# Kernel tuning notes

Measured on AMD Instinct MI355X. Metric: run time of the kernel, lower is better.

## Reference

```python
import jax, jax.numpy as jnp
import numpy as np

HEADS = 8

def setup_inputs() -> dict:
    key = jax.random.key(0)
    k1, k2 = jax.random.split(key)
    f_s = jax.random.normal(k1, (8, 256, 32, 32), dtype=jnp.float32)
    f_t = jax.random.normal(k2, (8, 256, 32, 32), dtype=jnp.float32)
    return {"f_s": f_s, "f_t": f_t}

def _to_tokens(x, heads):
    # 'b (h d) x y -> b h (x y) d'
    b, c, h, w = x.shape
    d = c // heads
    return x.reshape(b, heads, d, h * w).transpose(0, 1, 3, 2)

def reference(f_s, f_t):
    b, c, h, w = f_s.shape
    q = _to_tokens(f_s, HEADS)   # [b, H, n, d]
    k = _to_tokens(f_t, HEADS)
    v = _to_tokens(f_s, HEADS)
    # unscaled QK^T softmax V (faithful to source: no 1/sqrt(d) scaling)
    sim = jnp.einsum('bhid,bhjd->bhij', q, k)          # [b, H, n, n]
    attn = jax.nn.softmax(sim, axis=-1)
    out = jnp.einsum('bhij,bhjd->bhid', attn, v)       # [b, H, n, d]
    # 'b h (x y) d -> b (h d) x y'
    out = out.transpose(0, 1, 3, 2).reshape(b, c, h, w)
    loss = jnp.mean((out - f_t) ** 2)
    return loss
```

## Files before the change

kernel.cpp:

```cpp
#include <hip/hip_runtime.h>
#include <hip/hip_bf16.h>


typedef __attribute__((ext_vector_type(4))) float f32x4;
typedef __attribute__((ext_vector_type(16))) float f32x16;
typedef __attribute__((ext_vector_type(8))) short bf16x8;
typedef __attribute__((ext_vector_type(4))) unsigned u32x4;

#define KOFF 0
#define VOFF 65536
#define QOFF 131072
#define REDX 40960

__device__ __forceinline__ unsigned cvtpk(float a, float b) {
    unsigned r;
    asm("v_cvt_pk_bf16_f32 %0, %1, %2" : "=v"(r) : "v"(a), "v"(b));
    return r;
}
#define SWAP32(a, b) asm("v_permlane32_swap_b32 %0, %1" : "+v"(a), "+v"(b))

__device__ __forceinline__ float expv(float x) {
    float r;
    asm("v_exp_f32 %0, %1" : "=v"(r) : "v"(x));
    return r;
}

__global__ __launch_bounds__(512, 2)
void attn_mse_kernel(const float* __restrict__ fs, const float* __restrict__ ft,
                     float* __restrict__ out)
{
    __shared__ __align__(16) unsigned char smem[147456];

    const int tid  = threadIdx.x;
    const int lane = tid & 63;
    const int w    = tid >> 6;
    const int g    = lane >> 4;
    const int c    = lane & 15;
    const int il   = lane & 31;
    const int hi   = lane >> 5;

    const int bid  = blockIdx.x;
    const int pair = (bid & 7) * 8 + ((bid >> 3) & 7);
    const int q0   = (bid >> 6) * 256;

    const float* qb = fs + (size_t)pair * 32768;
    const float* kb = ft + (size_t)pair * 32768;

    const int p_ = c >> 2, jq = c & 3;
    const int dp = 4 * p_ + g;
    const int w0 = p_ * 64 + 16 * jq + 4 * (0 ^ p_) + g;
    const int w1 = p_ * 64 + 16 * jq + 4 * (1 ^ p_) + g;
    const int w2 = p_ * 64 + 16 * jq + 4 * (2 ^ p_) + g;
    const int w3 = p_ * 64 + 16 * jq + 4 * (3 ^ p_) + g;

    {
        const float sc = 1.44269504f;
        #pragma unroll
        for (int st = 0; st < 2; ++st) {
            const float* r0 = qb + (size_t)(2 * dp) * 1024 + (q0 + w * 32 + st * 16) + 4 * jq;
            const float4 a = *(const float4*)(r0);
            const float4 b = *(const float4*)(r0 + 1024);
            unsigned* dst = (unsigned*)(smem + QOFF + w * 2048 + st * 1024);
            dst[w0] = cvtpk(a.x * sc, b.x * sc);
            dst[w1] = cvtpk(a.y * sc, b.y * sc);
            dst[w2] = cvtpk(a.z * sc, b.z * sc);
            dst[w3] = cvtpk(a.w * sc, b.w * sc);
        }
    }
    const unsigned qsel = ((unsigned)(il >> 4) << 10) | (((unsigned)(il >> 2) & 3) << 6);
    const unsigned char* qbase = smem + QOFF + w * 2048 + qsel;
    const bf16x8 qfa = *(const bf16x8*)(qbase + ((hi << 8) | (((il & 3) ^ hi) << 4)));
    const bf16x8 qfb = *(const bf16x8*)(qbase + (((2 + hi) << 8) | (((il & 3) ^ (2 + hi)) << 4)));

    #pragma unroll
    for (int st = 0; st < 8; ++st) {
        const float* r0 = kb + (size_t)(2 * dp) * 1024 + (w * 128 + st * 16) + 4 * jq;
        const float4 a = *(const float4*)(r0);
        const float4 b = *(const float4*)(r0 + 1024);
        unsigned* dst = (unsigned*)(smem + KOFF + (w * 8 + st) * 1024);
        dst[w0] = cvtpk(a.x, b.x);
        dst[w1] = cvtpk(a.y, b.y);
        dst[w2] = cvtpk(a.z, b.z);
        dst[w3] = cvtpk(a.w, b.w);
    }
    {
        const int dv = w * 4 + g;
        #pragma unroll
        for (int tt = 0; tt < 16; ++tt) {
            const float4 vv = *(const float4*)(qb + (size_t)dv * 1024 + tt * 64 + 4 * c);
            const unsigned lo = cvtpk(vv.x, vv.y), hh = cvtpk(vv.z, vv.w);
            *(unsigned long long*)(smem + VOFF + tt * 4096 + dv * 128 +
                                   ((8 * c) ^ ((dv & 7) << 4))) =
                (unsigned long long)lo | ((unsigned long long)hh << 32);
        }
    }
    __syncthreads();

    f32x16 O, z16;
    #pragma unroll
    for (int r = 0; r < 16; ++r) { O[r] = 0.f; z16[r] = 0.f; }
    float lden = 0.f;

    #pragma unroll 1
    for (int t = 0; t < 16; ++t) {
        const int tile = (t + 2 * w) & 15;
        const unsigned char* vbase = smem + VOFF + tile * 4096 + il * 128;

        #pragma unroll
        for (int half = 0; half < 2; ++half) {
            const unsigned char* kbs = smem + KOFF + (tile * 2 + half) * 2048 + qsel;
            const bf16x8 ka0 = *(const bf16x8*)(kbs + ((hi << 8) | (((il & 3) ^ hi) << 4)));
            const bf16x8 ka1 = *(const bf16x8*)(kbs + (((2 + hi) << 8) | (((il & 3) ^ (2 + hi)) << 4)));
            f32x16 S;
            __builtin_amdgcn_s_setprio(1);
            S = __builtin_amdgcn_mfma_f32_32x32x16_bf16(ka0, qfa, z16, 0, 0, 0);
            S = __builtin_amdgcn_mfma_f32_32x32x16_bf16(ka1, qfb, S, 0, 0, 0);
            __builtin_amdgcn_s_setprio(0);

            #pragma unroll
            for (int r = 0; r < 16; ++r) S[r] = expv(S[r]);
            const float t0 = (S[0] + S[1]) + (S[2] + S[3]);
            const float t1 = (S[4] + S[5]) + (S[6] + S[7]);
            const float t2 = (S[8] + S[9]) + (S[10] + S[11]);
            const float t3 = (S[12] + S[13]) + (S[14] + S[15]);
            lden += (t0 + t1) + (t2 + t3);

            #pragma unroll
            for (int ks = 0; ks < 2; ++ks) {
                unsigned u0 = cvtpk(S[8 * ks + 0], S[8 * ks + 1]);
                unsigned u1 = cvtpk(S[8 * ks + 2], S[8 * ks + 3]);
                unsigned u2 = cvtpk(S[8 * ks + 4], S[8 * ks + 5]);
                unsigned u3 = cvtpk(S[8 * ks + 6], S[8 * ks + 7]);
                SWAP32(u0, u2); SWAP32(u1, u3);
                const u32x4 pw = {u0, u1, u2, u3};
                const bf16x8 pa = __builtin_bit_cast(bf16x8, pw);
                const unsigned col =
                    ((unsigned)(2 * (half * 32 + ks * 16 + 8 * hi))) ^ ((il & 7) << 4);
                const bf16x8 vbf = *(const bf16x8*)(vbase + col);
                __builtin_amdgcn_s_setprio(1);
                O = __builtin_amdgcn_mfma_f32_32x32x16_bf16(pa, vbf, O, 0, 0, 0);
                __builtin_amdgcn_s_setprio(0);
            }
        }
    }

    lden += __shfl_xor(lden, 32);
    const float li = 1.0f / lden;

    __syncthreads();
    float* ow = (float*)smem + w * 1104;
    #pragma unroll
    for (int r = 0; r < 16; ++r) {
        const int ir = (r & 3) + 8 * (r >> 2) + 4 * hi;
        ow[ir * 33 + il] = O[r];
    }
    const float* tvb = kb + (size_t)(q0 + w * 32) + il;
    float a0 = 0.f, a1 = 0.f;
    #pragma unroll
    for (int s = 0; s < 8; ++s) {
        const int d0 = 4 * s + hi, d1 = 4 * s + 2 + hi;
        const float e0 = ow[il * 33 + d0] * li - tvb[(size_t)d0 * 1024];
        const float e1 = ow[il * 33 + d1] * li - tvb[(size_t)d1 * 1024];
        a0 += e0 * e0; a1 += e1 * e1;
    }
    float acc = a0 + a1;
    #pragma unroll
    for (int off = 1; off < 64; off <<= 1) acc += __shfl_xor(acc, off);
    if (lane == 0) ((float*)(smem + REDX))[w] = acc;
    __syncthreads();
    if (tid == 0) {
        const float* lred = (const float*)(smem + REDX);
        float s = 0.f;
        #pragma unroll
        for (int i = 0; i < 8; ++i) s += lred[i];
        atomicAdd(out, s * (1.0f / 2097152.0f));
    }
}

extern "C" void kernel_launch(void* const* d_in, const int* in_sizes, int n_in,
                              void* d_out, int out_size, void* d_ws, size_t ws_size,
                              hipStream_t stream) {
    const float* fs = (const float*)d_in[0];
    const float* ft = (const float*)d_in[1];
    float* out = (float*)d_out;
    hipMemsetAsync(out, 0, sizeof(float), stream);
    attn_mse_kernel<<<dim3(256), dim3(512), 0, stream>>>(fs, ft, out);
}
```

Before: 27.50 us.

## Software-pipeline QK MFMA with exp/PV of previous sub-tile using double-buffered fragments

Restructures the attention main loop into a two-stage software pipeline. The K/V fragments for the next sub-tile are loaded from LDS, and its QK^T MFMA is issued while the previous sub-tile's exp, row-sum and PV MFMA run. This is meant to hide LDS latency and the MFMA-to-VALU dependency stalls by giving the scheduler independent work. In exchange it needs more live registers (two S accumulators and two fragment sets), which risks pressure at the 512-thread, 2-blocks-per-CU launch bound.

```diff
diff --git a/kernel.cpp b/kernel.cpp
--- a/kernel.cpp
+++ b/kernel.cpp
@@ -101,46 +101,67 @@
     for (int r = 0; r < 16; ++r) { O[r] = 0.f; z16[r] = 0.f; }
     float lden = 0.f;
 
+    bf16x8 kaA0, kaA1, vbA0, vbA1;
+    bf16x8 kaB0, kaB1, vbB0, vbB1;
+    f32x16 Sa, Sb;
+
+    const unsigned kb0off = (hi << 8) | (((il & 3) ^ hi) << 4);
+    const unsigned kb1off = ((2 + hi) << 8) | (((il & 3) ^ (2 + hi)) << 4);
+
+    auto LDFRAG = [&](int s, bf16x8& ka0, bf16x8& ka1, bf16x8& vb0, bf16x8& vb1) {
+        const int tile = ((s >> 1) + 2 * w) & 15;
+        const int half = s & 1;
+        const unsigned char* kbs = smem + KOFF + (tile * 2 + half) * 2048 + qsel;
+        ka0 = *(const bf16x8*)(kbs + kb0off);
+        ka1 = *(const bf16x8*)(kbs + kb1off);
+        const unsigned char* vbase = smem + VOFF + tile * 4096 + il * 128;
+        const unsigned col0 = ((unsigned)(2 * (half * 32 + 8 * hi))) ^ ((il & 7) << 4);
+        const unsigned col1 = ((unsigned)(2 * (half * 32 + 16 + 8 * hi))) ^ ((il & 7) << 4);
+        vb0 = *(const bf16x8*)(vbase + col0);
+        vb1 = *(const bf16x8*)(vbase + col1);
+    };
+    auto QK = [&](f32x16& S, const bf16x8& ka0, const bf16x8& ka1) {
+        __builtin_amdgcn_s_setprio(1);
+        S = __builtin_amdgcn_mfma_f32_32x32x16_bf16(ka0, qfa, z16, 0, 0, 0);
+        S = __builtin_amdgcn_mfma_f32_32x32x16_bf16(ka1, qfb, S, 0, 0, 0);
+        __builtin_amdgcn_s_setprio(0);
+    };
+    auto PVEXP = [&](f32x16& S, const bf16x8& vb0, const bf16x8& vb1) {
+        #pragma unroll
+        for (int r = 0; r < 16; ++r) S[r] = expv(S[r]);
+        const float t0 = (S[0] + S[1]) + (S[2] + S[3]);
+        const float t1 = (S[4] + S[5]) + (S[6] + S[7]);
+        const float t2 = (S[8] + S[9]) + (S[10] + S[11]);
+        const float t3 = (S[12] + S[13]) + (S[14] + S[15]);
+        lden += (t0 + t1) + (t2 + t3);
+        #pragma unroll
+        for (int ks = 0; ks < 2; ++ks) {
+            unsigned u0 = cvtpk(S[8 * ks + 0], S[8 * ks + 1]);
+            unsigned u1 = cvtpk(S[8 * ks + 2], S[8 * ks + 3]);
+            unsigned u2 = cvtpk(S[8 * ks + 4], S[8 * ks + 5]);
+            unsigned u3 = cvtpk(S[8 * ks + 6], S[8 * ks + 7]);
+            SWAP32(u0, u2); SWAP32(u1, u3);
+            const u32x4 pw = {u0, u1, u2, u3};
+            const bf16x8 pa = __builtin_bit_cast(bf16x8, pw);
+            __builtin_amdgcn_s_setprio(1);
+            O = __builtin_amdgcn_mfma_f32_32x32x16_bf16(pa, ks ? vb1 : vb0, O, 0, 0, 0);
+            __builtin_amdgcn_s_setprio(0);
+        }
+    };
+
+    LDFRAG(0, kaA0, kaA1, vbA0, vbA1);
+    QK(Sa, kaA0, kaA1);
     #pragma unroll 1
-    for (int t = 0; t < 16; ++t) {
-        const int tile = (t + 2 * w) & 15;
-        const unsigned char* vbase = smem + VOFF + tile * 4096 + il * 128;
-
-        #pragma unroll
-        for (int half = 0; half < 2; ++half) {
-            const unsigned char* kbs = smem + KOFF + (tile * 2 + half) * 2048 + qsel;
-            const bf16x8 ka0 = *(const bf16x8*)(kbs + ((hi << 8) | (((il & 3) ^ hi) << 4)));
-            const bf16x8 ka1 = *(const bf16x8*)(kbs + (((2 + hi) << 8) | (((il & 3) ^ (2 + hi)) << 4)));
-            f32x16 S;
-            __builtin_amdgcn_s_setprio(1);
-            S = __builtin_amdgcn_mfma_f32_32x32x16_bf16(ka0, qfa, z16, 0, 0, 0);
-            S = __builtin_amdgcn_mfma_f32_32x32x16_bf16(ka1, qfb, S, 0, 0, 0);
-            __builtin_amdgcn_s_setprio(0);
-
-            #pragma unroll
-            for (int r = 0; r < 16; ++r) S[r] = expv(S[r]);
-            const float t0 = (S[0] + S[1]) + (S[2] + S[3]);
-            const float t1 = (S[4] + S[5]) + (S[6] + S[7]);
-            const float t2 = (S[8] + S[9]) + (S[10] + S[11]);
-            const float t3 = (S[12] + S[13]) + (S[14] + S[15]);
-            lden += (t0 + t1) + (t2 + t3);
-
-            #pragma unroll
-            for (int ks = 0; ks < 2; ++ks) {
-                unsigned u0 = cvtpk(S[8 * ks + 0], S[8 * ks + 1]);
-                unsigned u1 = cvtpk(S[8 * ks + 2], S[8 * ks + 3]);
-                unsigned u2 = cvtpk(S[8 * ks + 4], S[8 * ks + 5]);
-                unsigned u3 = cvtpk(S[8 * ks + 6], S[8 * ks + 7]);
-                SWAP32(u0, u2); SWAP32(u1, u3);
-                const u32x4 pw = {u0, u1, u2, u3};
-                const bf16x8 pa = __builtin_bit_cast(bf16x8, pw);
-                const unsigned col =
-                    ((unsigned)(2 * (half * 32 + ks * 16 + 8 * hi))) ^ ((il & 7) << 4);
-                const bf16x8 vbf = *(const bf16x8*)(vbase + col);
-                __builtin_amdgcn_s_setprio(1);
-                O = __builtin_amdgcn_mfma_f32_32x32x16_bf16(pa, vbf, O, 0, 0, 0);
-                __builtin_amdgcn_s_setprio(0);
-            }
+    for (int s = 0; s < 32; s += 2) {
+        LDFRAG(s + 1, kaB0, kaB1, vbB0, vbB1);
+        PVEXP(Sa, vbA0, vbA1);
+        QK(Sb, kaB0, kaB1);
+        if (s + 2 < 32) {
+            LDFRAG(s + 2, kaA0, kaA1, vbA0, vbA1);
+            PVEXP(Sb, vbB0, vbB1);
+            QK(Sa, kaA0, kaA1);
+        } else {
+            PVEXP(Sb, vbB0, vbB1);
         }
     }
 
```

New measurement: 29.62 us. +7.7%, slower.
